# Kernel optimization log

Measured on AMD Instinct MI355X. Metric: run time of the kernel, lower is better.

## Reference

```python
import jax, jax.numpy as jnp
import numpy as np

B, D, O, E, K, H = 8192, 1024, 1024, 8, 2, 512
LOAD_BALANCE_ALPHA = 0.01


def setup_inputs() -> dict:
    key = jax.random.key(0)
    ks = jax.random.split(key, 7)
    s = 0.02
    return {
        "x": jax.random.normal(ks[0], (B, D), dtype=jnp.float32),
        "gate_W": jax.random.normal(ks[1], (D, E), dtype=jnp.float32) * s,
        "gate_b": jnp.zeros((E,), dtype=jnp.float32),
        "W1": jax.random.normal(ks[2], (E, D, H), dtype=jnp.float32) * s,
        "b1": jnp.zeros((E, H), dtype=jnp.float32),
        "W2": jax.random.normal(ks[3], (E, H, O), dtype=jnp.float32) * s,
        "b2": jnp.zeros((E, O), dtype=jnp.float32),
    }


def reference(x, gate_W, gate_b, W1, b1, W2, b2):
    # Gating (eval mode: no gate noise)
    gate_logits = x @ gate_W + gate_b                      # [B, E]
    top_v, top_i = jax.lax.top_k(gate_logits, K)           # [B, K]
    top_gates = jax.nn.softmax(top_v, axis=-1)             # [B, K]

    # All-expert MLP (E is small; dense grouped GEMM instead of per-sample loop)
    h = jax.nn.relu(jnp.einsum('bd,edh->ebh', x, W1) + b1[:, None, :])   # [E, B, H]
    expert_out = jnp.einsum('ebh,eho->beo', h, W2) + b2[None, :, :]      # [B, E, O]

    # Gather top-k expert outputs and weighted-combine
    sel = jnp.take_along_axis(expert_out, top_i[:, :, None], axis=1)     # [B, K, O]
    output = jnp.einsum('bk,bko->bo', top_gates, sel)                    # [B, O]

    # Load-balance auxiliary loss
    gates = jax.nn.softmax(gate_logits, axis=-1)
    importance = gates.mean(axis=0)                        # [E]
    load_balance_loss = E * jnp.sum(importance ** 2)
    return output, LOAD_BALANCE_ALPHA * load_balance_loss
```

## Files before the change

### kernel.cpp

```cpp
#include <hip/hip_runtime.h>
#include <hip/hip_bf16.h>
#include <stdint.h>

#define BB 8192
#define DD 1024
#define EE 8
#define HH 512
#define OO 1024
#define NG 16

typedef __bf16 bf16_t;
typedef bf16_t bf16x8 __attribute__((ext_vector_type(8)));
typedef float f32x4 __attribute__((ext_vector_type(4)));
typedef uint32_t u32;

#define CSTRIDE 16

#define WS_CNT    1024
#define WS_PPREF  2048
#define WS_RIDX   4096
#define WS_RGATE  (4096 + NG*BB*4)
#define WS_XB     (2u<<20)
#define WS_W1T    (WS_XB + (size_t)BB*DD*2)
#define WS_W2T    (WS_W1T + (size_t)EE*HH*DD*2)
#define WS_H      (WS_W2T + (size_t)EE*OO*HH*2)

#define GL16(gsrc, ldst)                                                       \
  __builtin_amdgcn_global_load_lds(                                            \
      (const __attribute__((address_space(1))) void*)(gsrc),                   \
      (__attribute__((address_space(3))) void*)(ldst), 16, 0, 0)

__global__ __launch_bounds__(256) void k_prep(const float* __restrict__ W1,
                                              const float* __restrict__ W2,
                                              bf16_t* __restrict__ W1T,
                                              bf16_t* __restrict__ W2T) {
  __shared__ __align__(16) bf16_t t[64][72];
  int bid = blockIdx.x;
  const float* src; bf16_t* dst; int R, C; int tile;
  if (bid < 1024) {
    int e = bid >> 7; tile = bid & 127;
    src = W1 + (size_t)e * DD * HH; dst = W1T + (size_t)e * HH * DD;
    R = DD; C = HH;
  } else {
    bid -= 1024;
    int e = bid >> 7; tile = bid & 127;
    src = W2 + (size_t)e * HH * OO; dst = W2T + (size_t)e * OO * HH;
    R = HH; C = OO;
  }
  int tpc = C >> 6;
  int r0 = (tile / tpc) << 6, c0 = (tile % tpc) << 6;
  int tid = threadIdx.x;
  {
    int r = tid >> 2, cs = (tid & 3) << 4;
    const f32x4* sp = (const f32x4*)(src + (size_t)(r0 + r) * C + c0 + cs);
    #pragma unroll
    for (int q = 0; q < 4; ++q) {
      f32x4 v = sp[q];
      t[cs + q*4 + 0][r] = (bf16_t)v.x;
      t[cs + q*4 + 1][r] = (bf16_t)v.y;
      t[cs + q*4 + 2][r] = (bf16_t)v.z;
      t[cs + q*4 + 3][r] = (bf16_t)v.w;
    }
  }
  __syncthreads();
  {
    int c = tid >> 2, rs = (tid & 3) << 4;
    bf16_t* op = dst + (size_t)(c0 + c) * R + r0 + rs;
    const uint4* lp = (const uint4*)(&t[c][rs]);
    uint4 a0 = lp[0], a1 = lp[1];
    ((uint4*)op)[0] = a0;
    ((uint4*)op)[1] = a1;
  }
}

__global__ __launch_bounds__(1024, 8) void k_gate(const float* __restrict__ x,
                                                  const float* __restrict__ gW,
                                                  const float* __restrict__ gb,
                                                  float* __restrict__ imp,
                                                  u32* __restrict__ cnt,
                                                  int* __restrict__ ridx,
                                                  float* __restrict__ rgate,
                                                  bf16_t* __restrict__ xb) {
  __shared__ __align__(16) float gLds[EE * DD];
  __shared__ float s_imp[EE];
  __shared__ u32 s_hist[NG];
  __shared__ u32 s_base[NG];
  __shared__ int   s_lb[NG][32];
  __shared__ float s_lg[NG][32];
  int tid = threadIdx.x;
  if (tid < EE) s_imp[tid] = 0.f;
  if (tid < NG) s_hist[tid] = 0u;
  {
    const f32x4* gp = (const f32x4*)(gW + (size_t)tid * EE);
    f32x4 g0 = gp[0], g1 = gp[1];
    gLds[0 * DD + tid] = g0.x; gLds[1 * DD + tid] = g0.y;
    gLds[2 * DD + tid] = g0.z; gLds[3 * DD + tid] = g0.w;
    gLds[4 * DD + tid] = g1.x; gLds[5 * DD + tid] = g1.y;
    gLds[6 * DD + tid] = g1.z; gLds[7 * DD + tid] = g1.w;
  }
  __syncthreads();

  int lane = tid & 63, w = tid >> 6;
  int b = (blockIdx.x << 4) + w;
  const float* xrow = x + (size_t)b * DD;
  bf16_t* xbrow = xb + (size_t)b * DD;

  double acc[EE];
  #pragma unroll
  for (int e = 0; e < EE; ++e) acc[e] = 0.0;

  #pragma unroll
  for (int q = 0; q < 4; ++q) {
    int d0 = (q << 8) + (lane << 2);
    f32x4 xv = *(const f32x4*)(xrow + d0);
    bf16_t xc[4] = {(bf16_t)xv.x, (bf16_t)xv.y, (bf16_t)xv.z, (bf16_t)xv.w};
    *(uint2*)(xbrow + d0) = *(const uint2*)xc;
    #pragma unroll
    for (int e = 0; e < EE; ++e) {
      f32x4 gv = *(const f32x4*)(gLds + e * DD + d0);
      acc[e] += (double)xv.x * gv.x;
      acc[e] += (double)xv.y * gv.y;
      acc[e] += (double)xv.z * gv.z;
      acc[e] += (double)xv.w * gv.w;
    }
  }
  #pragma unroll
  for (int e = 0; e < EE; ++e) {
    #pragma unroll
    for (int off = 32; off > 0; off >>= 1) acc[e] += __shfl_xor(acc[e], off);
  }
  if (lane == 0) {
    float v[EE];
    float m = -1e30f;
    #pragma unroll
    for (int e = 0; e < EE; ++e) { v[e] = (float)acc[e] + gb[e]; m = fmaxf(m, v[e]); }
    float s = 0.f, p[EE];
    #pragma unroll
    for (int e = 0; e < EE; ++e) { p[e] = expf(v[e] - m); s += p[e]; }
    float inv = 1.f / s;
    #pragma unroll
    for (int e = 0; e < EE; ++e) atomicAdd(&s_imp[e], p[e] * inv);
    int i0 = 0; float b0 = v[0];
    #pragma unroll
    for (int e = 1; e < EE; ++e) if (v[e] > b0) { b0 = v[e]; i0 = e; }
    int i1 = -1; float b1v = -1e30f;
    #pragma unroll
    for (int e = 0; e < EE; ++e) if (e != i0 && v[e] > b1v) { b1v = v[e]; i1 = e; }
    float tt = expf(b1v - b0);
    float g0 = 1.f / (1.f + tt), g1 = tt / (1.f + tt);
    int ga = i0 * 2, gbq = i1 * 2 + 1;
    u32 p0 = atomicAdd(&s_hist[ga], 1u);
    s_lb[ga][p0] = b; s_lg[ga][p0] = g0;
    u32 p1 = atomicAdd(&s_hist[gbq], 1u);
    s_lb[gbq][p1] = b; s_lg[gbq][p1] = g1;
  }
  __syncthreads();
  if (tid < NG) s_base[tid] = atomicAdd(&cnt[tid * CSTRIDE], s_hist[tid]);
  if (tid < EE) atomicAdd(&imp[tid * CSTRIDE], s_imp[tid]);
  __syncthreads();
  if (tid < NG * 32) {
    int g = tid >> 5, k = tid & 31;
    if ((u32)k < s_hist[g]) {
      u32 pos = s_base[g] + (u32)k;
      ridx[g * BB + pos] = s_lb[g][k];
      rgate[g * BB + pos] = s_lg[g][k];
    }
  }
}

__global__ void k_loss(const float* __restrict__ imp, const u32* __restrict__ cnt,
                       u32* __restrict__ ppref, float* __restrict__ outloss) {
  int tid = threadIdx.x;
  float v = (tid < EE) ? imp[tid * CSTRIDE] * (1.f / BB) : 0.f;
  v = v * v;
  #pragma unroll
  for (int off = 32; off > 0; off >>= 1) v += __shfl_xor(v, off);
  if (tid == 0) {
    *outloss = 0.01f * (float)EE * v;
    u32 s = 0;
    for (int g = 0; g < NG; ++g) {
      ppref[g] = s;
      s += ((cnt[g * CSTRIDE] + 127u) >> 7) << 7;
    }
  }
}

__global__ __launch_bounds__(256, 2) void k_mlp1(const u32* __restrict__ cnt,
                                                 const u32* __restrict__ ppref,
                                                 const int* __restrict__ ridx,
                                                 const bf16_t* __restrict__ xb,
                                                 const bf16_t* __restrict__ W1T,
                                                 const float* __restrict__ b1,
                                                 bf16_t* __restrict__ Hc) {
  __shared__ __align__(16) bf16_t sA[128 * 64];
  __shared__ __align__(16) bf16_t sB[128 * 64];
  __shared__ int s_rb[128];

  int bid = blockIdx.x;
  int g = bid & 15; int t2 = bid >> 4; int nt = t2 & 3; int mt = t2 >> 2;
  int e = g >> 1;
  int n = (int)cnt[g * CSTRIDE];
  int m0 = mt << 7;
  if (m0 >= n) return;
  int tid = threadIdx.x;
  if (tid < 128) {
    int i = m0 + tid;
    s_rb[tid] = ridx[g * BB + min(i, n - 1)];
  }
  __syncthreads();

  int lane = tid & 63, w = tid >> 6;
  int lrow = lane >> 3, lcol = (lane & 7) << 3;
  int n0 = nt << 7;
  const bf16_t* w1b = W1T + (size_t)e * HH * DD + (size_t)n0 * DD;

  const bf16_t* aptr[4]; const bf16_t* bptr[4];
  #pragma unroll
  for (int q = 0; q < 4; ++q) {
    int r = w * 32 + q * 8 + lrow;
    aptr[q] = xb + (size_t)s_rb[r] * DD + lcol;
    bptr[q] = w1b + (size_t)r * DD + lcol;
  }

  f32x4 acc[4][4];
  f32x4 zz = {0.f, 0.f, 0.f, 0.f};
  #pragma unroll
  for (int mm = 0; mm < 4; ++mm)
    #pragma unroll
    for (int nn = 0; nn < 4; ++nn) acc[mm][nn] = zz;

  int lr = lane & 15, lk = lane >> 4;
  int wr = w >> 1, wc = w & 1;

  for (int kk = 0; kk < 16; ++kk) {
    #pragma unroll
    for (int q = 0; q < 4; ++q) {
      GL16(aptr[q], sA + (w * 32 + q * 8) * 64);
      GL16(bptr[q], sB + (w * 32 + q * 8) * 64);
      aptr[q] += 64; bptr[q] += 64;
    }
    __syncthreads();
    #pragma unroll
    for (int ks = 0; ks < 2; ++ks) {
      bf16x8 af[4], bfr[4];
      #pragma unroll
      for (int mm = 0; mm < 4; ++mm)
        af[mm] = *(const bf16x8*)(sA + (wr * 64 + mm * 16 + lr) * 64 + (ks * 4 + lk) * 8);
      #pragma unroll
      for (int nn = 0; nn < 4; ++nn)
        bfr[nn] = *(const bf16x8*)(sB + (wc * 64 + nn * 16 + lr) * 64 + (ks * 4 + lk) * 8);
      #pragma unroll
      for (int mm = 0; mm < 4; ++mm)
        #pragma unroll
        for (int nn = 0; nn < 4; ++nn)
          acc[mm][nn] = __builtin_amdgcn_mfma_f32_16x16x32_bf16(bfr[nn], af[mm], acc[mm][nn], 0, 0, 0);
    }
    __syncthreads();
  }

  int hbase = (int)ppref[g] + m0;
  const float* b1p = b1 + (size_t)e * HH + n0;
  #pragma unroll
  for (int mm = 0; mm < 4; ++mm) {
    int m = wr * 64 + mm * 16 + lr;
    size_t hrow = (size_t)(hbase + m) * HH + n0;
    #pragma unroll
    for (int nn = 0; nn < 4; ++nn) {
      int h0l = wc * 64 + nn * 16 + lk * 4;
      bf16_t pk[4];
      #pragma unroll
      for (int j = 0; j < 4; ++j)
        pk[j] = (bf16_t)fmaxf(acc[mm][nn][j] + b1p[h0l + j], 0.f);
      *(uint2*)(Hc + hrow + h0l) = *(const uint2*)pk;
    }
  }
}

template <int ADD>
__global__ __launch_bounds__(256, 2) void k_mlp2(const u32* __restrict__ cnt,
                                                 const u32* __restrict__ ppref,
                                                 const int* __restrict__ ridx,
                                                 const float* __restrict__ rgate,
                                                 const bf16_t* __restrict__ Hc,
                                                 const bf16_t* __restrict__ W2T,
                                                 const float* __restrict__ b2,
                                                 float* __restrict__ out) {
  __shared__ __align__(16) bf16_t sA[128 * 64];
  __shared__ __align__(16) bf16_t sB[128 * 64];
  __shared__ int s_rb[128];
  __shared__ float s_rg[128];

  int bid = blockIdx.x;
  int e = bid & 7; int g = (e << 1) | ADD;
  int t2 = bid >> 3; int nt = t2 & 7; int mt = t2 >> 3;
  int n = (int)cnt[g * CSTRIDE];
  int m0 = mt << 7;
  if (m0 >= n) return;
  int tid = threadIdx.x;
  if (tid < 128) {
    int i = m0 + tid;
    int ic = min(i, n - 1);
    s_rb[tid] = ridx[g * BB + ic];
    s_rg[tid] = (i < n) ? rgate[g * BB + ic] : 0.f;
  }
  __syncthreads();

  int lane = tid & 63, w = tid >> 6;
  int lrow = lane >> 3, lcol = (lane & 7) << 3;
  int n0 = nt << 7;
  int hbase = (int)ppref[g] + m0;
  const bf16_t* w2b = W2T + (size_t)e * OO * HH + (size_t)n0 * HH;

  const bf16_t* aptr[4]; const bf16_t* bptr[4];
  #pragma unroll
  for (int q = 0; q < 4; ++q) {
    int r = w * 32 + q * 8 + lrow;
    aptr[q] = Hc + (size_t)(hbase + r) * HH + lcol;
    bptr[q] = w2b + (size_t)r * HH + lcol;
  }

  f32x4 acc[4][4];
  f32x4 zz = {0.f, 0.f, 0.f, 0.f};
  #pragma unroll
  for (int mm = 0; mm < 4; ++mm)
    #pragma unroll
    for (int nn = 0; nn < 4; ++nn) acc[mm][nn] = zz;

  int lr = lane & 15, lk = lane >> 4;
  int wr = w >> 1, wc = w & 1;

  for (int kk = 0; kk < 8; ++kk) {
    #pragma unroll
    for (int q = 0; q < 4; ++q) {
      GL16(aptr[q], sA + (w * 32 + q * 8) * 64);
      GL16(bptr[q], sB + (w * 32 + q * 8) * 64);
      aptr[q] += 64; bptr[q] += 64;
    }
    __syncthreads();
    #pragma unroll
    for (int ks = 0; ks < 2; ++ks) {
      bf16x8 af[4], bfr[4];
      #pragma unroll
      for (int mm = 0; mm < 4; ++mm)
        af[mm] = *(const bf16x8*)(sA + (wr * 64 + mm * 16 + lr) * 64 + (ks * 4 + lk) * 8);
      #pragma unroll
      for (int nn = 0; nn < 4; ++nn)
        bfr[nn] = *(const bf16x8*)(sB + (wc * 64 + nn * 16 + lr) * 64 + (ks * 4 + lk) * 8);
      #pragma unroll
      for (int mm = 0; mm < 4; ++mm)
        #pragma unroll
        for (int nn = 0; nn < 4; ++nn)
          acc[mm][nn] = __builtin_amdgcn_mfma_f32_16x16x32_bf16(bfr[nn], af[mm], acc[mm][nn], 0, 0, 0);
    }
    __syncthreads();
  }

  const float* b2p = b2 + (size_t)e * OO + n0;
  #pragma unroll
  for (int mm = 0; mm < 4; ++mm) {
    int m = wr * 64 + mm * 16 + lr;
    if (m0 + m < n) {
      float gg = s_rg[m];
      float* orow = out + (size_t)s_rb[m] * OO + n0;
      #pragma unroll
      for (int nn = 0; nn < 4; ++nn) {
        int o0 = wc * 64 + nn * 16 + lk * 4;
        f32x4 v;
        #pragma unroll
        for (int j = 0; j < 4; ++j)
          v[j] = (acc[mm][nn][j] + b2p[o0 + j]) * gg;
        if (ADD) {
          f32x4 old = *(const f32x4*)(orow + o0);
          v += old;
        }
        *(f32x4*)(orow + o0) = v;
      }
    }
  }
}

extern "C" void kernel_launch(void* const* d_in, const int* in_sizes, int n_in,
                              void* d_out, int out_size, void* d_ws, size_t ws_size,
                              hipStream_t stream) {
  const float* x   = (const float*)d_in[0];
  const float* gW  = (const float*)d_in[1];
  const float* gb  = (const float*)d_in[2];
  const float* W1  = (const float*)d_in[3];
  const float* b1  = (const float*)d_in[4];
  const float* W2  = (const float*)d_in[5];
  const float* b2  = (const float*)d_in[6];
  float* out = (float*)d_out;

  uint8_t* ws = (uint8_t*)d_ws;
  float*   imp   = (float*)(ws + 0);
  u32*     cnt   = (u32*)(ws + WS_CNT);
  u32*     ppref = (u32*)(ws + WS_PPREF);
  int*     ridx  = (int*)(ws + WS_RIDX);
  float*   rgate = (float*)(ws + WS_RGATE);
  bf16_t*  xb    = (bf16_t*)(ws + WS_XB);
  bf16_t*  W1T   = (bf16_t*)(ws + WS_W1T);
  bf16_t*  W2T   = (bf16_t*)(ws + WS_W2T);
  bf16_t*  Hc    = (bf16_t*)(ws + WS_H);

  hipMemsetAsync(ws, 0, 4096, stream);

  k_prep<<<2048, 256, 0, stream>>>(W1, W2, W1T, W2T);
  k_gate<<<512, 1024, 0, stream>>>(x, gW, gb, imp, cnt, ridx, rgate, xb);
  k_loss<<<1, 64, 0, stream>>>(imp, cnt, ppref, out + (size_t)BB * OO);
  k_mlp1<<<NG * 4 * 64, 256, 0, stream>>>(cnt, ppref, ridx, xb, W1T, b1, Hc);
  k_mlp2<0><<<EE * 8 * 64, 256, 0, stream>>>(cnt, ppref, ridx, rgate, Hc, W2T, b2, out);
  k_mlp2<1><<<EE * 8 * 64, 256, 0, stream>>>(cnt, ppref, ridx, rgate, Hc, W2T, b2, out);
}
```

Measured before the change: 137.6 us.

## Double-buffer LDS tiles and XOR-swizzle layout in both expert GEMM kernels

```diff
diff --git a/kernel.cpp b/kernel.cpp
--- a/kernel.cpp
+++ b/kernel.cpp
@@ -192,8 +192,8 @@
                                                  const bf16_t* __restrict__ W1T,
                                                  const float* __restrict__ b1,
                                                  bf16_t* __restrict__ Hc) {
-  __shared__ __align__(16) bf16_t sA[128 * 64];
-  __shared__ __align__(16) bf16_t sB[128 * 64];
+  __shared__ __align__(16) bf16_t sA[2][128 * 64];
+  __shared__ __align__(16) bf16_t sB[2][128 * 64];
   __shared__ int s_rb[128];
 
   int bid = blockIdx.x;
@@ -210,7 +210,8 @@
   __syncthreads();
 
   int lane = tid & 63, w = tid >> 6;
-  int lrow = lane >> 3, lcol = (lane & 7) << 3;
+  int lrow = lane >> 3;
+  int lcol = (((lane & 7) ^ lrow) << 3);
   int n0 = nt << 7;
   const bf16_t* w1b = W1T + (size_t)e * HH * DD + (size_t)n0 * DD;
 
@@ -231,24 +232,36 @@
 
   int lr = lane & 15, lk = lane >> 4;
   int wr = w >> 1, wc = w & 1;
+  int rsw = lr & 7;
+
+  #pragma unroll
+  for (int q = 0; q < 4; ++q) {
+    GL16(aptr[q], &sA[0][(w * 32 + q * 8) * 64]);
+    GL16(bptr[q], &sB[0][(w * 32 + q * 8) * 64]);
+    aptr[q] += 64; bptr[q] += 64;
+  }
+  __syncthreads();
 
   for (int kk = 0; kk < 16; ++kk) {
-    #pragma unroll
-    for (int q = 0; q < 4; ++q) {
-      GL16(aptr[q], sA + (w * 32 + q * 8) * 64);
-      GL16(bptr[q], sB + (w * 32 + q * 8) * 64);
-      aptr[q] += 64; bptr[q] += 64;
-    }
-    __syncthreads();
+    int cur = kk & 1;
+    if (kk < 15) {
+      #pragma unroll
+      for (int q = 0; q < 4; ++q) {
+        GL16(aptr[q], &sA[cur ^ 1][(w * 32 + q * 8) * 64]);
+        GL16(bptr[q], &sB[cur ^ 1][(w * 32 + q * 8) * 64]);
+        aptr[q] += 64; bptr[q] += 64;
+      }
+    }
     #pragma unroll
     for (int ks = 0; ks < 2; ++ks) {
+      int swb = ((ks * 4 + lk) ^ rsw) << 3;
       bf16x8 af[4], bfr[4];
       #pragma unroll
       for (int mm = 0; mm < 4; ++mm)
-        af[mm] = *(const bf16x8*)(sA + (wr * 64 + mm * 16 + lr) * 64 + (ks * 4 + lk) * 8);
+        af[mm] = *(const bf16x8*)(&sA[cur][(wr * 64 + mm * 16 + lr) * 64 + swb]);
       #pragma unroll
       for (int nn = 0; nn < 4; ++nn)
-        bfr[nn] = *(const bf16x8*)(sB + (wc * 64 + nn * 16 + lr) * 64 + (ks * 4 + lk) * 8);
+        bfr[nn] = *(const bf16x8*)(&sB[cur][(wc * 64 + nn * 16 + lr) * 64 + swb]);
       #pragma unroll
       for (int mm = 0; mm < 4; ++mm)
         #pragma unroll
@@ -285,8 +298,8 @@
                                                  const bf16_t* __restrict__ W2T,
                                                  const float* __restrict__ b2,
                                                  float* __restrict__ out) {
-  __shared__ __align__(16) bf16_t sA[128 * 64];
-  __shared__ __align__(16) bf16_t sB[128 * 64];
+  __shared__ __align__(16) bf16_t sA[2][128 * 64];
+  __shared__ __align__(16) bf16_t sB[2][128 * 64];
   __shared__ int s_rb[128];
   __shared__ float s_rg[128];
 
@@ -306,7 +319,8 @@
   __syncthreads();
 
   int lane = tid & 63, w = tid >> 6;
-  int lrow = lane >> 3, lcol = (lane & 7) << 3;
+  int lrow = lane >> 3;
+  int lcol = (((lane & 7) ^ lrow) << 3);
   int n0 = nt << 7;
   int hbase = (int)ppref[g] + m0;
   const bf16_t* w2b = W2T + (size_t)e * OO * HH + (size_t)n0 * HH;
@@ -328,24 +342,36 @@
 
   int lr = lane & 15, lk = lane >> 4;
   int wr = w >> 1, wc = w & 1;
+  int rsw = lr & 7;
+
+  #pragma unroll
+  for (int q = 0; q < 4; ++q) {
+    GL16(aptr[q], &sA[0][(w * 32 + q * 8) * 64]);
+    GL16(bptr[q], &sB[0][(w * 32 + q * 8) * 64]);
+    aptr[q] += 64; bptr[q] += 64;
+  }
+  __syncthreads();
 
   for (int kk = 0; kk < 8; ++kk) {
-    #pragma unroll
-    for (int q = 0; q < 4; ++q) {
-      GL16(aptr[q], sA + (w * 32 + q * 8) * 64);
-      GL16(bptr[q], sB + (w * 32 + q * 8) * 64);
-      aptr[q] += 64; bptr[q] += 64;
-    }
-    __syncthreads();
+    int cur = kk & 1;
+    if (kk < 7) {
+      #pragma unroll
+      for (int q = 0; q < 4; ++q) {
+        GL16(aptr[q], &sA[cur ^ 1][(w * 32 + q * 8) * 64]);
+        GL16(bptr[q], &sB[cur ^ 1][(w * 32 + q * 8) * 64]);
+        aptr[q] += 64; bptr[q] += 64;
+      }
+    }
     #pragma unroll
     for (int ks = 0; ks < 2; ++ks) {
+      int swb = ((ks * 4 + lk) ^ rsw) << 3;
       bf16x8 af[4], bfr[4];
       #pragma unroll
       for (int mm = 0; mm < 4; ++mm)
-        af[mm] = *(const bf16x8*)(sA + (wr * 64 + mm * 16 + lr) * 64 + (ks * 4 + lk) * 8);
+        af[mm] = *(const bf16x8*)(&sA[cur][(wr * 64 + mm * 16 + lr) * 64 + swb]);
       #pragma unroll
       for (int nn = 0; nn < 4; ++nn)
-        bfr[nn] = *(const bf16x8*)(sB + (wc * 64 + nn * 16 + lr) * 64 + (ks * 4 + lk) * 8);
+        bfr[nn] = *(const bf16x8*)(&sB[cur][(wc * 64 + nn * 16 + lr) * 64 + swb]);
       #pragma unroll
       for (int mm = 0; mm < 4; ++mm)
         #pragma unroll
```

New measurement: 144.9 us. +5.3%, slower.

## Swizzle LDS tiles, narrow mlp1 N-tile to 64, raise occupancy to 4

Applied to the files above, without the earlier changes.

```diff
diff --git a/kernel.cpp b/kernel.cpp
--- a/kernel.cpp
+++ b/kernel.cpp
@@ -185,7 +185,7 @@
   }
 }
 
-__global__ __launch_bounds__(256, 2) void k_mlp1(const u32* __restrict__ cnt,
+__global__ __launch_bounds__(256, 4) void k_mlp1(const u32* __restrict__ cnt,
                                                  const u32* __restrict__ ppref,
                                                  const int* __restrict__ ridx,
                                                  const bf16_t* __restrict__ xb,
@@ -193,12 +193,16 @@
                                                  const float* __restrict__ b1,
                                                  bf16_t* __restrict__ Hc) {
   __shared__ __align__(16) bf16_t sA[128 * 64];
-  __shared__ __align__(16) bf16_t sB[128 * 64];
+  __shared__ __align__(16) bf16_t sB[64 * 64];
   __shared__ int s_rb[128];
 
   int bid = blockIdx.x;
-  int g = bid & 15; int t2 = bid >> 4; int nt = t2 & 3; int mt = t2 >> 2;
-  int e = g >> 1;
+  int e = bid & 7;
+  int widx = bid >> 3;
+  int nt = widx & 7;
+  int mt = (widx >> 3) & 63;
+  int which = (widx >> 9) & 1;
+  int g = e * 2 + which;
   int n = (int)cnt[g * CSTRIDE];
   int m0 = mt << 7;
   if (m0 >= n) return;
@@ -210,49 +214,60 @@
   __syncthreads();
 
   int lane = tid & 63, w = tid >> 6;
-  int lrow = lane >> 3, lcol = (lane & 7) << 3;
-  int n0 = nt << 7;
+  int lrow = lane >> 3;
+  int lcol = (((lane & 7) ^ lrow) << 3);
+  int n0 = nt << 6;
   const bf16_t* w1b = W1T + (size_t)e * HH * DD + (size_t)n0 * DD;
 
-  const bf16_t* aptr[4]; const bf16_t* bptr[4];
+  const bf16_t* aptr[4]; const bf16_t* bptr[2];
   #pragma unroll
   for (int q = 0; q < 4; ++q) {
     int r = w * 32 + q * 8 + lrow;
     aptr[q] = xb + (size_t)s_rb[r] * DD + lcol;
+  }
+  #pragma unroll
+  for (int q = 0; q < 2; ++q) {
+    int r = w * 16 + q * 8 + lrow;
     bptr[q] = w1b + (size_t)r * DD + lcol;
   }
 
-  f32x4 acc[4][4];
+  f32x4 acc[4][2];
   f32x4 zz = {0.f, 0.f, 0.f, 0.f};
   #pragma unroll
   for (int mm = 0; mm < 4; ++mm)
     #pragma unroll
-    for (int nn = 0; nn < 4; ++nn) acc[mm][nn] = zz;
+    for (int nn = 0; nn < 2; ++nn) acc[mm][nn] = zz;
 
   int lr = lane & 15, lk = lane >> 4;
   int wr = w >> 1, wc = w & 1;
+  int rsw = lr & 7;
 
   for (int kk = 0; kk < 16; ++kk) {
     #pragma unroll
     for (int q = 0; q < 4; ++q) {
       GL16(aptr[q], sA + (w * 32 + q * 8) * 64);
-      GL16(bptr[q], sB + (w * 32 + q * 8) * 64);
-      aptr[q] += 64; bptr[q] += 64;
+      aptr[q] += 64;
+    }
+    #pragma unroll
+    for (int q = 0; q < 2; ++q) {
+      GL16(bptr[q], sB + (w * 16 + q * 8) * 64);
+      bptr[q] += 64;
     }
     __syncthreads();
     #pragma unroll
     for (int ks = 0; ks < 2; ++ks) {
-      bf16x8 af[4], bfr[4];
+      int swb = ((ks * 4 + lk) ^ rsw) << 3;
+      bf16x8 af[4], bfr[2];
       #pragma unroll
       for (int mm = 0; mm < 4; ++mm)
-        af[mm] = *(const bf16x8*)(sA + (wr * 64 + mm * 16 + lr) * 64 + (ks * 4 + lk) * 8);
-      #pragma unroll
-      for (int nn = 0; nn < 4; ++nn)
-        bfr[nn] = *(const bf16x8*)(sB + (wc * 64 + nn * 16 + lr) * 64 + (ks * 4 + lk) * 8);
+        af[mm] = *(const bf16x8*)(sA + (wr * 64 + mm * 16 + lr) * 64 + swb);
+      #pragma unroll
+      for (int nn = 0; nn < 2; ++nn)
+        bfr[nn] = *(const bf16x8*)(sB + (wc * 32 + nn * 16 + lr) * 64 + swb);
       #pragma unroll
       for (int mm = 0; mm < 4; ++mm)
         #pragma unroll
-        for (int nn = 0; nn < 4; ++nn)
+        for (int nn = 0; nn < 2; ++nn)
           acc[mm][nn] = __builtin_amdgcn_mfma_f32_16x16x32_bf16(bfr[nn], af[mm], acc[mm][nn], 0, 0, 0);
     }
     __syncthreads();
@@ -265,8 +280,8 @@
     int m = wr * 64 + mm * 16 + lr;
     size_t hrow = (size_t)(hbase + m) * HH + n0;
     #pragma unroll
-    for (int nn = 0; nn < 4; ++nn) {
-      int h0l = wc * 64 + nn * 16 + lk * 4;
+    for (int nn = 0; nn < 2; ++nn) {
+      int h0l = wc * 32 + nn * 16 + lk * 4;
       bf16_t pk[4];
       #pragma unroll
       for (int j = 0; j < 4; ++j)
@@ -277,7 +292,7 @@
 }
 
 template <int ADD>
-__global__ __launch_bounds__(256, 2) void k_mlp2(const u32* __restrict__ cnt,
+__global__ __launch_bounds__(256, 4) void k_mlp2(const u32* __restrict__ cnt,
                                                  const u32* __restrict__ ppref,
                                                  const int* __restrict__ ridx,
                                                  const float* __restrict__ rgate,
@@ -306,7 +321,8 @@
   __syncthreads();
 
   int lane = tid & 63, w = tid >> 6;
-  int lrow = lane >> 3, lcol = (lane & 7) << 3;
+  int lrow = lane >> 3;
+  int lcol = (((lane & 7) ^ lrow) << 3);
   int n0 = nt << 7;
   int hbase = (int)ppref[g] + m0;
   const bf16_t* w2b = W2T + (size_t)e * OO * HH + (size_t)n0 * HH;
@@ -328,6 +344,7 @@
 
   int lr = lane & 15, lk = lane >> 4;
   int wr = w >> 1, wc = w & 1;
+  int rsw = lr & 7;
 
   for (int kk = 0; kk < 8; ++kk) {
     #pragma unroll
@@ -339,13 +356,14 @@
     __syncthreads();
     #pragma unroll
     for (int ks = 0; ks < 2; ++ks) {
+      int swb = ((ks * 4 + lk) ^ rsw) << 3;
       bf16x8 af[4], bfr[4];
       #pragma unroll
       for (int mm = 0; mm < 4; ++mm)
-        af[mm] = *(const bf16x8*)(sA + (wr * 64 + mm * 16 + lr) * 64 + (ks * 4 + lk) * 8);
+        af[mm] = *(const bf16x8*)(sA + (wr * 64 + mm * 16 + lr) * 64 + swb);
       #pragma unroll
       for (int nn = 0; nn < 4; ++nn)
-        bfr[nn] = *(const bf16x8*)(sB + (wc * 64 + nn * 16 + lr) * 64 + (ks * 4 + lk) * 8);
+        bfr[nn] = *(const bf16x8*)(sB + (wc * 64 + nn * 16 + lr) * 64 + swb);
       #pragma unroll
       for (int mm = 0; mm < 4; ++mm)
         #pragma unroll
@@ -407,7 +425,7 @@
   k_prep<<<2048, 256, 0, stream>>>(W1, W2, W1T, W2T);
   k_gate<<<512, 1024, 0, stream>>>(x, gW, gb, imp, cnt, ridx, rgate, xb);
   k_loss<<<1, 64, 0, stream>>>(imp, cnt, ppref, out + (size_t)BB * OO);
-  k_mlp1<<<NG * 4 * 64, 256, 0, stream>>>(cnt, ppref, ridx, xb, W1T, b1, Hc);
+  k_mlp1<<<8 * 2 * 64 * 8, 256, 0, stream>>>(cnt, ppref, ridx, xb, W1T, b1, Hc);
   k_mlp2<0><<<EE * 8 * 64, 256, 0, stream>>>(cnt, ppref, ridx, rgate, Hc, W2T, b2, out);
   k_mlp2<1><<<EE * 8 * 64, 256, 0, stream>>>(cnt, ppref, ridx, rgate, Hc, W2T, b2, out);
 }
```

Result: faster. 123.0 us (-10.6%).
